# Performance work log

Hardware: AMD Instinct MI355X
Metric: run time of the kernel (lower is better)

The kernel has to match this reference:

```python
import jax, jax.numpy as jnp
import numpy as np

T, B, I, H, E, C = 256, 64, 1024, 1024, 4, 128
STDV = 1.0 / np.sqrt(H)


def setup_inputs() -> dict:
    key = jax.random.key(0)
    ks = jax.random.split(key, 8)
    x_seq = jax.random.normal(ks[0], (T, B, I), dtype=jnp.float32)
    h0 = jnp.zeros((1, B, H), dtype=jnp.float32)
    c0 = jnp.zeros((1, B, H), dtype=jnp.float32)
    coef = jax.random.uniform(ks[1], (B, E), dtype=jnp.float32)
    # expert params (uniform(-stdv, stdv) init as in the torch module)
    u = lambda k, shp: jax.random.uniform(k, shp, dtype=jnp.float32, minval=-STDV, maxval=STDV)
    Wi = u(ks[2], (E, 4 * H, I))
    bi = u(ks[3], (E, 4 * H))
    Wh = u(ks[4], (E, 4 * H, H))
    bh = u(ks[5], (E, 4 * H))
    Wo = u(ks[6], (E, C, H))
    bo = u(ks[7], (E, C))
    return {"x_seq": x_seq, "h0": h0, "c0": c0, "coef": coef,
            "Wi": Wi, "bi": bi, "Wh": Wh, "bh": bh, "Wo": Wo, "bo": bo}


def reference(x_seq, h0, c0, coef, Wi, bi, Wh, bh, Wo, bo):
    # MoO with IDGate == per-sample convex combination of expert linear outputs,
    # which equals a linear layer with per-sample mixed weights.
    # Precompute mixed input projections for all timesteps: [T,B,4H]
    xi = jnp.einsum('tbi,eoi,be->tbo', x_seq, Wi, coef) + coef @ bi
    # Per-sample mixed hidden weights: [B,4H,H] and bias [B,4H]
    Whm = jnp.einsum('eoi,be->boi', Wh, coef)
    bhm = coef @ bh

    def step(carry, xg):
        h, c = carry
        gates = xg + jnp.einsum('bi,boi->bo', h, Whm) + bhm  # [B,4H]
        ig, fg, gg, og = jnp.split(gates, 4, axis=-1)  # i,f,g,o order as in torch chunk
        c = jax.nn.sigmoid(fg) * c + jax.nn.sigmoid(ig) * jnp.tanh(gg)
        h = jax.nn.sigmoid(og) * jnp.tanh(c)
        return (h, c), h

    (hT, cT), hs = jax.lax.scan(step, (h0[0], c0[0]), xi)  # hs: [T,B,H]
    # h2o: mixed output projection (activation is identity, dropout p=0)
    out = jnp.einsum('tbh,ech,be->tbc', hs, Wo, coef) + coef @ bo  # [T,B,C]
    return out, hT[None], cT[None]
```

## Files before the change

kernel.cpp:

```cpp
#include <hip/hip_runtime.h>
#include <hip/hip_fp16.h>
#include <cstdint>

#define T_  256
#define B_  64
#define I_  1024
#define H_  1024
#define E_  4
#define C_  128
#define G4  4096

typedef _Float16 f16;
typedef _Float16 f16x2 __attribute__((ext_vector_type(2)));
typedef _Float16 f16x8 __attribute__((ext_vector_type(8)));
typedef float    f32x4 __attribute__((ext_vector_type(4)));

__device__ __forceinline__ float sigmoidf_(float x) { return 1.f / (1.f + __expf(-x)); }

union pk2 { uint32_t u; f16x2 h; };

__global__ void k_f32_to_f16(const float* __restrict__ src, f16* __restrict__ dst, int n8) {
    int i = blockIdx.x * blockDim.x + threadIdx.x;
    int stride = gridDim.x * blockDim.x;
    for (; i < n8; i += stride) {
        const float4* s = reinterpret_cast<const float4*>(src) + (size_t)i * 2;
        float4 a = s[0], b = s[1];
        f16x8 v = { (f16)a.x, (f16)a.y, (f16)a.z, (f16)a.w,
                    (f16)b.x, (f16)b.y, (f16)b.z, (f16)b.w };
        *reinterpret_cast<f16x8*>(dst + (size_t)i * 8) = v;
    }
}

__global__ void k_mix_biases(const float* __restrict__ coef, const float* __restrict__ bi,
                             const float* __restrict__ bh, const float* __restrict__ bo,
                             float* __restrict__ gbias, float* __restrict__ bom) {
    int idx = blockIdx.x * blockDim.x + threadIdx.x;
    int stride = gridDim.x * blockDim.x;
    for (int i = idx; i < B_ * G4; i += stride) {
        int b = i >> 12, o = i & (G4 - 1);
        float s = 0.f;
#pragma unroll
        for (int e = 0; e < 4; ++e) s += coef[b * 4 + e] * (bi[e * G4 + o] + bh[e * G4 + o]);
        gbias[i] = s;
    }
    for (int i = idx; i < B_ * C_; i += stride) {
        int b = i >> 7, c = i & (C_ - 1);
        float s = 0.f;
#pragma unroll
        for (int e = 0; e < 4; ++e) s += coef[b * 4 + e] * bo[e * C_ + c];
        bom[i] = s;
    }
}

__global__ void k_init_h0h(const float* __restrict__ h0, f16* __restrict__ h0h) {
    int i = blockIdx.x * blockDim.x + threadIdx.x;
    if (i < B_ * H_) h0h[i] = (f16)h0[i];
}

template<bool XF16, bool WF16>
__global__ __launch_bounds__(256, 1) void k_xi_gemm(
        const f16* __restrict__ xh, const float* __restrict__ xf,
        const f16* __restrict__ Wih, const float* __restrict__ Wif,
        const float* __restrict__ coef, const float* __restrict__ gbias,
        f16* __restrict__ xi) {
    __shared__ f16 As[256 * 72];
    __shared__ f16 Bs[128 * 72];
    const int nt = blockIdx.x;
    const int b  = blockIdx.y;
    const int tid = threadIdx.x;
    const int lane = tid & 63, wave = tid >> 6;
    const int wr = wave >> 1, wc = wave & 1;

    float cf[4];
#pragma unroll
    for (int e = 0; e < 4; ++e) cf[e] = coef[b * 4 + e];

    f32x4 acc[8][4];
#pragma unroll
    for (int mi = 0; mi < 8; ++mi)
#pragma unroll
        for (int ni = 0; ni < 4; ++ni) acc[mi][ni] = 0.f;

    for (int kk = 0; kk < I_; kk += 64) {
        __syncthreads();
#pragma unroll
        for (int it = 0; it < 8; ++it) {
            int chunk = it * 256 + tid;
            int row = chunk >> 3, c8 = chunk & 7;
            if constexpr (XF16) {
                *reinterpret_cast<f16x8*>(&As[row * 72 + c8 * 8]) =
                    *reinterpret_cast<const f16x8*>(&xh[((size_t)row * B_ + b) * I_ + kk + c8 * 8]);
            } else {
                const float4* p = reinterpret_cast<const float4*>(&xf[((size_t)row * B_ + b) * I_ + kk + c8 * 8]);
                float4 a = p[0], bq = p[1];
                f16x8 v = { (f16)a.x, (f16)a.y, (f16)a.z, (f16)a.w,
                            (f16)bq.x, (f16)bq.y, (f16)bq.z, (f16)bq.w };
                *reinterpret_cast<f16x8*>(&As[row * 72 + c8 * 8]) = v;
            }
        }
#pragma unroll
        for (int it = 0; it < 4; ++it) {
            int chunk = it * 256 + tid;
            int n = chunk >> 3, c8 = chunk & 7;
            if constexpr (WF16) {
                size_t base = ((size_t)(nt * 128 + n)) * I_ + kk + c8 * 8;
                f16 c0 = (f16)cf[0], c1 = (f16)cf[1], c2 = (f16)cf[2], c3 = (f16)cf[3];
                f16x8 w0 = *reinterpret_cast<const f16x8*>(&Wih[base]);
                f16x8 w1 = *reinterpret_cast<const f16x8*>(&Wih[base + (size_t)1 * G4 * I_]);
                f16x8 w2 = *reinterpret_cast<const f16x8*>(&Wih[base + (size_t)2 * G4 * I_]);
                f16x8 w3 = *reinterpret_cast<const f16x8*>(&Wih[base + (size_t)3 * G4 * I_]);
                f16x8 m = w0 * c0 + w1 * c1 + w2 * c2 + w3 * c3;
                *reinterpret_cast<f16x8*>(&Bs[n * 72 + c8 * 8]) = m;
            } else {
                size_t base = ((size_t)(nt * 128 + n)) * I_ + kk + c8 * 8;
                float m[8];
#pragma unroll
                for (int j = 0; j < 8; ++j) m[j] = 0.f;
#pragma unroll
                for (int e = 0; e < 4; ++e) {
                    const float4* p = reinterpret_cast<const float4*>(&Wif[base + (size_t)e * G4 * I_]);
                    float4 a = p[0], bq = p[1];
                    m[0] += cf[e] * a.x;  m[1] += cf[e] * a.y;
                    m[2] += cf[e] * a.z;  m[3] += cf[e] * a.w;
                    m[4] += cf[e] * bq.x; m[5] += cf[e] * bq.y;
                    m[6] += cf[e] * bq.z; m[7] += cf[e] * bq.w;
                }
                f16x8 v = { (f16)m[0], (f16)m[1], (f16)m[2], (f16)m[3],
                            (f16)m[4], (f16)m[5], (f16)m[6], (f16)m[7] };
                *reinterpret_cast<f16x8*>(&Bs[n * 72 + c8 * 8]) = v;
            }
        }
        __syncthreads();
#pragma unroll
        for (int ks = 0; ks < 2; ++ks) {
            int ko = ks * 32 + (lane >> 4) * 8;
            f16x8 a[8], bb[4];
#pragma unroll
            for (int mi = 0; mi < 8; ++mi)
                a[mi] = *reinterpret_cast<const f16x8*>(&As[(wr * 128 + mi * 16 + (lane & 15)) * 72 + ko]);
#pragma unroll
            for (int ni = 0; ni < 4; ++ni)
                bb[ni] = *reinterpret_cast<const f16x8*>(&Bs[(wc * 64 + ni * 16 + (lane & 15)) * 72 + ko]);
#pragma unroll
            for (int mi = 0; mi < 8; ++mi)
#pragma unroll
                for (int ni = 0; ni < 4; ++ni)
                    acc[mi][ni] = __builtin_amdgcn_mfma_f32_16x16x32_f16(a[mi], bb[ni], acc[mi][ni], 0, 0, 0);
        }
    }
#pragma unroll
    for (int mi = 0; mi < 8; ++mi)
#pragma unroll
        for (int ni = 0; ni < 4; ++ni)
#pragma unroll
            for (int j = 0; j < 4; ++j) {
                int t = wr * 128 + mi * 16 + (lane >> 4) * 4 + j;
                int o = nt * 128 + wc * 64 + ni * 16 + (lane & 15);
                float v = acc[mi][ni][j] + gbias[b * G4 + o];
                xi[((size_t)t * B_ + b) * G4 + o] = (f16)v;
            }
}

__device__ __forceinline__ void grid_barrier3(int* __restrict__ arr, int* __restrict__ go,
                                              int t, int bid) {
    __syncthreads();
    const int tid = threadIdx.x;
    if (bid == 0) {
        if (tid >= 1 && tid < 256) {
            while (__hip_atomic_load(&arr[t * 256 + tid], __ATOMIC_RELAXED,
                                     __HIP_MEMORY_SCOPE_AGENT) == 0)
                __builtin_amdgcn_s_sleep(1);
        }
        __syncthreads();
        if (tid == 0)
            __hip_atomic_store(&go[t * 512 + 511], 1, __ATOMIC_RELEASE,
                               __HIP_MEMORY_SCOPE_AGENT);
        __syncthreads();
        if (tid < 32)
            __hip_atomic_store(&go[t * 512 + tid * 16], 1, __ATOMIC_RELAXED,
                               __HIP_MEMORY_SCOPE_AGENT);
        __syncthreads();
    } else {
        if (tid == 0) {
            __hip_atomic_store(&arr[t * 256 + bid], 1, __ATOMIC_RELEASE,
                               __HIP_MEMORY_SCOPE_AGENT);
            while (__hip_atomic_load(&go[t * 512 + (bid >> 3) * 16], __ATOMIC_RELAXED,
                                     __HIP_MEMORY_SCOPE_AGENT) == 0)
                __builtin_amdgcn_s_sleep(1);
        }
        __builtin_amdgcn_sched_barrier(0);
        __syncthreads();
    }
}

#define POOL_SZ  148480
#define AS0_OFF  131072
#define AS1_OFF  (131072 + 8192)
#define GL_OFF   131072

#define BF(KC, KS) (*reinterpret_cast<const f16x8*>(pool + wrow + (KC) * 128 + (((KS) * 64 + koff) ^ swz)))

#define PRE(KC, PF) PF = *reinterpret_cast<const f16x8*>(&hprev[(size_t)sr * hstr + (KC) * 64 + soct * 8]);

#define AFR(AOFF, AROW, KS) (*reinterpret_cast<const f16x8*>(pool + (AOFF) + (AROW) + (((KS) * 64 + koff) ^ swz)))

#define MM4(ROFF) \
    acc0 = __builtin_amdgcn_mfma_f32_16x16x32_f16(AFR(ROFF, arow0, 0), bq0, acc0, 0, 0, 0); \
    acc1 = __builtin_amdgcn_mfma_f32_16x16x32_f16(AFR(ROFF, arow1, 0), bq0, acc1, 0, 0, 0); \
    acc0 = __builtin_amdgcn_mfma_f32_16x16x32_f16(AFR(ROFF, arow0, 1), bq1, acc0, 0, 0, 0); \
    acc1 = __builtin_amdgcn_mfma_f32_16x16x32_f16(AFR(ROFF, arow1, 1), bq1, acc1, 0, 0, 0);

#define KSTP(KC, ROFF, WOFF, PFW, PFL) { \
    const f16x8 bq0 = BF(KC, 0), bq1 = BF(KC, 1); \
    PRE((KC) + 8, PFL); \
    MM4(ROFF); \
    *reinterpret_cast<f16x8*>(pool + (WOFF) + sdst) = PFW; \
    __syncthreads(); \
}
#define KST(KC, ROFF, WOFF, PFW) { \
    const f16x8 bq0 = BF(KC, 0), bq1 = BF(KC, 1); \
    MM4(ROFF); \
    *reinterpret_cast<f16x8*>(pool + (WOFF) + sdst) = PFW; \
    __syncthreads(); \
}

__global__ __launch_bounds__(512, 1) void k_rec_persist(
        const float* __restrict__ Wh, const f16* __restrict__ h0h,
        const float* __restrict__ c0, f16* xi, const float* __restrict__ coef,
        float* __restrict__ out, int* __restrict__ arr, int* __restrict__ go) {
    __shared__ __attribute__((aligned(16))) char pool[POOL_SZ];
    float* gl = reinterpret_cast<float*>(pool + GL_OFF);

    const int bid = blockIdx.x;
    const int jb = ((bid & 7) << 5) | (bid >> 3);
    const int tid = threadIdx.x, lane = tid & 63, w = tid >> 6;
    const int ex = w & 3, mh = w >> 2;
    const int l15 = lane & 15, hi8 = (lane >> 4) * 8;

    for (int i = tid; i < 8192; i += 512) {
        int r = i >> 7, oct = i & 127;
        int e = r >> 4, g = (r >> 2) & 3, c = r & 3;
        const float* src = &Wh[((size_t)e * G4 + g * H_ + jb * 4 + c) * H_ + oct * 8];
        float4 f0 = *reinterpret_cast<const float4*>(src);
        float4 f1 = *reinterpret_cast<const float4*>(src + 4);
        f16x8 v = { (f16)f0.x, (f16)f0.y, (f16)f0.z, (f16)f0.w,
                    (f16)f1.x, (f16)f1.y, (f16)f1.z, (f16)f1.w };
        int db = r * 2048 + ((oct * 16) ^ ((r & 7) << 4));
        *reinterpret_cast<f16x8*>(pool + db) = v;
    }

    const int bb = tid >> 1, pr = tid & 1;
    const int cp0 = jb * 4 + pr * 2;
    float c_reg0 = 0.f, c_reg1 = 0.f;
    float4 cf4 = {0.f, 0.f, 0.f, 0.f};
    if (tid < 128) {
        c_reg0 = c0[bb * H_ + cp0];
        c_reg1 = c0[bb * H_ + cp0 + 1];
        cf4 = *reinterpret_cast<const float4*>(&coef[bb * 4]);
    }

    const int swz   = (l15 & 7) << 4;
    const int koff  = hi8 * 2;
    const int wrow  = (ex * 16 + l15) * 2048;
    const int arow0 = (mh * 32 + l15) * 128;
    const int arow1 = arow0 + 16 * 128;
    const int sr = tid >> 3, soct = tid & 7;
    const int sdst = sr * 128 + ((soct * 16) ^ ((sr & 7) << 4));

    __syncthreads();

    float xgc0a = 0.f, xgc0b = 0.f, xgc1a = 0.f, xgc1b = 0.f;
    float xgc2a = 0.f, xgc2b = 0.f, xgc3a = 0.f, xgc3b = 0.f;
    if (tid < 128) {
        const f16* xp = &xi[((size_t)0 * B_ + bb) * G4 + cp0];
        pk2 p0; p0.u = __hip_atomic_load(reinterpret_cast<const uint32_t*>(xp),
                                         __ATOMIC_RELAXED, __HIP_MEMORY_SCOPE_AGENT);
        xgc0a = (float)p0.h.x; xgc0b = (float)p0.h.y;
        f16x2 g1 = *reinterpret_cast<const f16x2*>(xp + H_);
        f16x2 g2 = *reinterpret_cast<const f16x2*>(xp + 2 * H_);
        f16x2 g3 = *reinterpret_cast<const f16x2*>(xp + 3 * H_);
        xgc1a = (float)g1.x; xgc1b = (float)g1.y;
        xgc2a = (float)g2.x; xgc2b = (float)g2.y;
        xgc3a = (float)g3.x; xgc3b = (float)g3.y;
    }

    for (int t = 0; t < T_; ++t) {
        const f16* hprev = (t == 0) ? h0h : (xi + (size_t)(t - 1) * B_ * G4);
        const size_t hstr = (t == 0) ? (size_t)H_ : (size_t)G4;

        f16x8 pfa, pfb, pfc, pfd, pfe, pff, pfg, pfh;
        PRE(0, pfa) PRE(1, pfb) PRE(2, pfc) PRE(3, pfd)
        PRE(4, pfe) PRE(5, pff) PRE(6, pfg) PRE(7, pfh)

        float xgn0a = 0.f, xgn0b = 0.f, xgn1a = 0.f, xgn1b = 0.f;
        float xgn2a = 0.f, xgn2b = 0.f, xgn3a = 0.f, xgn3b = 0.f;
        if (t + 1 < T_ && tid < 128) {
            const f16* xq = &xi[((size_t)(t + 1) * B_ + bb) * G4 + cp0];
            pk2 p0; p0.u = __hip_atomic_load(reinterpret_cast<const uint32_t*>(xq),
                                             __ATOMIC_RELAXED, __HIP_MEMORY_SCOPE_AGENT);
            xgn0a = (float)p0.h.x; xgn0b = (float)p0.h.y;
            f16x2 g1 = *reinterpret_cast<const f16x2*>(xq + H_);
            f16x2 g2 = *reinterpret_cast<const f16x2*>(xq + 2 * H_);
            f16x2 g3 = *reinterpret_cast<const f16x2*>(xq + 3 * H_);
            xgn1a = (float)g1.x; xgn1b = (float)g1.y;
            xgn2a = (float)g2.x; xgn2b = (float)g2.y;
            xgn3a = (float)g3.x; xgn3b = (float)g3.y;
        }

        *reinterpret_cast<f16x8*>(pool + AS0_OFF + sdst) = pfa;
        f32x4 acc0 = {0.f, 0.f, 0.f, 0.f}, acc1 = {0.f, 0.f, 0.f, 0.f};
        __syncthreads();

        KSTP(0,  AS0_OFF, AS1_OFF, pfb, pfa)
        KSTP(1,  AS1_OFF, AS0_OFF, pfc, pfb)
        KSTP(2,  AS0_OFF, AS1_OFF, pfd, pfc)
        KSTP(3,  AS1_OFF, AS0_OFF, pfe, pfd)
        KSTP(4,  AS0_OFF, AS1_OFF, pff, pfe)
        KSTP(5,  AS1_OFF, AS0_OFF, pfg, pff)
        KSTP(6,  AS0_OFF, AS1_OFF, pfh, pfg)
        KSTP(7,  AS1_OFF, AS0_OFF, pfa, pfh)
        KST(8,   AS0_OFF, AS1_OFF, pfb)
        KST(9,   AS1_OFF, AS0_OFF, pfc)
        KST(10,  AS0_OFF, AS1_OFF, pfd)
        KST(11,  AS1_OFF, AS0_OFF, pfe)
        KST(12,  AS0_OFF, AS1_OFF, pff)
        KST(13,  AS1_OFF, AS0_OFF, pfg)
        KST(14,  AS0_OFF, AS1_OFF, pfh)
        {
            const f16x8 bq0 = BF(15, 0), bq1 = BF(15, 1);
            MM4(AS1_OFF);
            __syncthreads();
        }

#pragma unroll
        for (int j = 0; j < 4; ++j) {
            int r0 = mh * 32 + (lane >> 4) * 4 + j;
            gl[(ex * 64 + r0) * 17 + l15]      = acc0[j];
            gl[(ex * 64 + r0 + 16) * 17 + l15] = acc1[j];
        }
        __syncthreads();

        if (tid < 128) {
            float ga[4], gb[4];
#pragma unroll
            for (int g = 0; g < 4; ++g) {
                int nn = g * 4 + pr * 2;
                ga[g] = cf4.x * gl[(0 * 64 + bb) * 17 + nn] +
                        cf4.y * gl[(1 * 64 + bb) * 17 + nn] +
                        cf4.z * gl[(2 * 64 + bb) * 17 + nn] +
                        cf4.w * gl[(3 * 64 + bb) * 17 + nn];
                gb[g] = cf4.x * gl[(0 * 64 + bb) * 17 + nn + 1] +
                        cf4.y * gl[(1 * 64 + bb) * 17 + nn + 1] +
                        cf4.z * gl[(2 * 64 + bb) * 17 + nn + 1] +
                        cf4.w * gl[(3 * 64 + bb) * 17 + nn + 1];
            }
            ga[0] += xgc0a; ga[1] += xgc1a; ga[2] += xgc2a; ga[3] += xgc3a;
            gb[0] += xgc0b; gb[1] += xgc1b; gb[2] += xgc2b; gb[3] += xgc3b;
            float cn0 = sigmoidf_(ga[1]) * c_reg0 + sigmoidf_(ga[0]) * tanhf(ga[2]);
            float hn0 = sigmoidf_(ga[3]) * tanhf(cn0);
            float cn1 = sigmoidf_(gb[1]) * c_reg1 + sigmoidf_(gb[0]) * tanhf(gb[2]);
            float hn1 = sigmoidf_(gb[3]) * tanhf(cn1);
            c_reg0 = cn0; c_reg1 = cn1;
            pk2 st; st.h.x = (f16)hn0; st.h.y = (f16)hn1;
            __hip_atomic_store(reinterpret_cast<uint32_t*>(&xi[((size_t)t * B_ + bb) * G4 + cp0]),
                               st.u, __ATOMIC_RELAXED, __HIP_MEMORY_SCOPE_AGENT);
            if (t == T_ - 1) {
                out[(size_t)T_ * B_ * C_ + bb * H_ + cp0]     = hn0;
                out[(size_t)T_ * B_ * C_ + bb * H_ + cp0 + 1] = hn1;
                out[(size_t)T_ * B_ * C_ + B_ * H_ + bb * H_ + cp0]     = cn0;
                out[(size_t)T_ * B_ * C_ + B_ * H_ + bb * H_ + cp0 + 1] = cn1;
            }
        }
        xgc0a = xgn0a; xgc0b = xgn0b; xgc1a = xgn1a; xgc1b = xgn1b;
        xgc2a = xgn2a; xgc2b = xgn2b; xgc3a = xgn3a; xgc3b = xgn3b;
        if (t != T_ - 1) grid_barrier3(arr, go, t, bid);
    }
}

__global__ __launch_bounds__(256, 1) void k_out_gemm(
        const f16* __restrict__ hs, const f16* __restrict__ Woh,
        const float* __restrict__ coef, const float* __restrict__ bom,
        float* __restrict__ out) {
    __shared__ f16 As[64 * 72];
    __shared__ f16 Bs[256 * 72];
    __shared__ float cfs[64][4];
    const int nt = blockIdx.x;
    const int t  = blockIdx.y;
    const int tid = threadIdx.x, lane = tid & 63, w = tid >> 6;
    cfs[tid >> 2][tid & 3] = coef[tid];

    f32x4 acc[4][4];
#pragma unroll
    for (int e = 0; e < 4; ++e)
#pragma unroll
        for (int mi = 0; mi < 4; ++mi) acc[e][mi] = 0.f;

    for (int kk = 0; kk < H_; kk += 64) {
        __syncthreads();
#pragma unroll
        for (int it = 0; it < 2; ++it) {
            int chunk = it * 256 + tid;
            int row = chunk >> 3, c8 = chunk & 7;
            *reinterpret_cast<f16x8*>(&As[row * 72 + c8 * 8]) =
                *reinterpret_cast<const f16x8*>(&hs[((size_t)t * B_ + row) * G4 + kk + c8 * 8]);
        }
#pragma unroll
        for (int it = 0; it < 8; ++it) {
            int chunk = it * 256 + tid;
            int r = chunk >> 3, c8 = chunk & 7;
            int e = r >> 6, nn = r & 63;
            size_t grow = (size_t)e * C_ + nt * 64 + nn;
            *reinterpret_cast<f16x8*>(&Bs[r * 72 + c8 * 8]) =
                *reinterpret_cast<const f16x8*>(&Woh[grow * H_ + kk + c8 * 8]);
        }
        __syncthreads();
#pragma unroll
        for (int ks = 0; ks < 2; ++ks) {
            int ko = ks * 32 + (lane >> 4) * 8;
            f16x8 a[4];
#pragma unroll
            for (int mi = 0; mi < 4; ++mi)
                a[mi] = *reinterpret_cast<const f16x8*>(&As[(mi * 16 + (lane & 15)) * 72 + ko]);
#pragma unroll
            for (int e = 0; e < 4; ++e) {
                f16x8 bf = *reinterpret_cast<const f16x8*>(&Bs[(e * 64 + w * 16 + (lane & 15)) * 72 + ko]);
#pragma unroll
                for (int mi = 0; mi < 4; ++mi)
                    acc[e][mi] = __builtin_amdgcn_mfma_f32_16x16x32_f16(a[mi], bf, acc[e][mi], 0, 0, 0);
            }
        }
    }
#pragma unroll
    for (int mi = 0; mi < 4; ++mi)
#pragma unroll
        for (int j = 0; j < 4; ++j) {
            int bb = mi * 16 + (lane >> 4) * 4 + j;
            int cc = nt * 64 + w * 16 + (lane & 15);
            float v = cfs[bb][0] * acc[0][mi][j] + cfs[bb][1] * acc[1][mi][j] +
                      cfs[bb][2] * acc[2][mi][j] + cfs[bb][3] * acc[3][mi][j];
            v += bom[bb * C_ + cc];
            out[((size_t)t * B_ + bb) * C_ + cc] = v;
        }
}

extern "C" void kernel_launch(void* const* d_in, const int* in_sizes, int n_in,
                              void* d_out, int out_size, void* d_ws, size_t ws_size,
                              hipStream_t stream) {
    const float* x    = (const float*)d_in[0];
    const float* h0   = (const float*)d_in[1];
    const float* c0   = (const float*)d_in[2];
    const float* coef = (const float*)d_in[3];
    const float* Wi   = (const float*)d_in[4];
    const float* bi   = (const float*)d_in[5];
    const float* Wh   = (const float*)d_in[6];
    const float* bh   = (const float*)d_in[7];
    const float* Wo   = (const float*)d_in[8];
    const float* bo   = (const float*)d_in[9];
    float* out = (float*)d_out;

    char* base = (char*)d_ws;
    size_t off = 0;
    auto carve = [&](size_t bytes) -> char* {
        char* r = base + off;
        off = (off + bytes + 255) & ~(size_t)255;
        return r;
    };
    const size_t SZ_XI  = (size_t)T_ * B_ * G4 * 2;
    const size_t SZ_WOH = (size_t)E_ * C_ * H_ * 2;
    const size_t SZ_ARR = (size_t)T_ * 256 * 4;
    const size_t SZ_GO  = (size_t)T_ * 512 * 4;
    const size_t SZ_WIH = (size_t)E_ * G4 * I_ * 2;
    const size_t SZ_XH  = (size_t)T_ * B_ * I_ * 2;

    f16*   xi     = (f16*)carve(SZ_XI);
    f16*   Woh    = (f16*)carve(SZ_WOH);
    f16*   h0h    = (f16*)carve((size_t)B_ * H_ * 2);
    float* gbias  = (float*)carve((size_t)B_ * G4 * 4);
    float* bom    = (float*)carve((size_t)B_ * C_ * 4);
    int*   arr    = (int*)carve(SZ_ARR);
    int*   go     = (int*)carve(SZ_GO);

    f16* Wih = nullptr;
    f16* xh  = nullptr;
    if (off + SZ_WIH + 256 <= ws_size) Wih = (f16*)carve(SZ_WIH);
    if (Wih && off + SZ_XH + 256 <= ws_size) xh = (f16*)carve(SZ_XH);
    (void)in_sizes; (void)n_in; (void)out_size;

    hipMemsetAsync(arr, 0, SZ_ARR, stream);
    hipMemsetAsync(go, 0, SZ_GO, stream);

    if (xh)  k_f32_to_f16<<<2048, 256, 0, stream>>>(x,  xh,  (T_ * B_ * I_) / 8);
    if (Wih) k_f32_to_f16<<<2048, 256, 0, stream>>>(Wi, Wih, (E_ * G4 * I_) / 8);
    k_f32_to_f16<<<512,  256, 0, stream>>>(Wo, Woh, (E_ * C_ * H_) / 8);
    k_mix_biases<<<512, 256, 0, stream>>>(coef, bi, bh, bo, gbias, bom);
    k_init_h0h<<<(B_ * H_ + 255) / 256, 256, 0, stream>>>(h0, h0h);

    dim3 gx(32, 64);
    if (xh)
        k_xi_gemm<true,  true ><<<gx, 256, 0, stream>>>(xh, nullptr, Wih, nullptr, coef, gbias, xi);
    else if (Wih)
        k_xi_gemm<false, true ><<<gx, 256, 0, stream>>>(nullptr, x, Wih, nullptr, coef, gbias, xi);
    else
        k_xi_gemm<false, false><<<gx, 256, 0, stream>>>(nullptr, x, nullptr, Wi, coef, gbias, xi);

    {
        void* args[] = { (void*)&Wh, (void*)&h0h, (void*)&c0, (void*)&xi,
                         (void*)&coef, (void*)&out, (void*)&arr, (void*)&go };
        hipLaunchCooperativeKernel((const void*)k_rec_persist, dim3(256), dim3(512),
                                   args, 0, stream);
    }

    dim3 go_(2, 256);
    k_out_gemm<<<go_, 256, 0, stream>>>(xi, Woh, coef, bom, out);
}
```

Baseline: 2.688 ms.

## Replace global grid barrier with per-tile dataflow flags polled during k-loop

Removes the centralized two-level grid barrier between timesteps. Each block now publishes its own arrival flag. The last block of each 16-block tile to see its whole tile complete raises per-tile go flags, replicated into 16 lines. Consumers wait only for the tiles covering the h chunks they are about to load, polling inside the k-loop so compute on early chunks overlaps with late producers. The prefetch depth shrinks from 8 to 4 chunks to match the staggered waits. This adds more flag traffic and memory-ordering risk, since relaxed atomics are used without explicit release/acquire fences.

```diff
diff --git a/kernel.cpp b/kernel.cpp
--- a/kernel.cpp
+++ b/kernel.cpp
@@ -161,47 +161,13 @@
             }
 }
 
-__device__ __forceinline__ void grid_barrier3(int* __restrict__ arr, int* __restrict__ go,
-                                              int t, int bid) {
-    __syncthreads();
-    const int tid = threadIdx.x;
-    if (bid == 0) {
-        if (tid >= 1 && tid < 256) {
-            while (__hip_atomic_load(&arr[t * 256 + tid], __ATOMIC_RELAXED,
-                                     __HIP_MEMORY_SCOPE_AGENT) == 0)
-                __builtin_amdgcn_s_sleep(1);
-        }
-        __syncthreads();
-        if (tid == 0)
-            __hip_atomic_store(&go[t * 512 + 511], 1, __ATOMIC_RELEASE,
-                               __HIP_MEMORY_SCOPE_AGENT);
-        __syncthreads();
-        if (tid < 32)
-            __hip_atomic_store(&go[t * 512 + tid * 16], 1, __ATOMIC_RELAXED,
-                               __HIP_MEMORY_SCOPE_AGENT);
-        __syncthreads();
-    } else {
-        if (tid == 0) {
-            __hip_atomic_store(&arr[t * 256 + bid], 1, __ATOMIC_RELEASE,
-                               __HIP_MEMORY_SCOPE_AGENT);
-            while (__hip_atomic_load(&go[t * 512 + (bid >> 3) * 16], __ATOMIC_RELAXED,
-                                     __HIP_MEMORY_SCOPE_AGENT) == 0)
-                __builtin_amdgcn_s_sleep(1);
-        }
-        __builtin_amdgcn_sched_barrier(0);
-        __syncthreads();
-    }
-}
-
 #define POOL_SZ  148480
 #define AS0_OFF  131072
 #define AS1_OFF  (131072 + 8192)
 #define GL_OFF   131072
 
 #define BF(KC, KS) (*reinterpret_cast<const f16x8*>(pool + wrow + (KC) * 128 + (((KS) * 64 + koff) ^ swz)))
-
 #define PRE(KC, PF) PF = *reinterpret_cast<const f16x8*>(&hprev[(size_t)sr * hstr + (KC) * 64 + soct * 8]);
-
 #define AFR(AOFF, AROW, KS) (*reinterpret_cast<const f16x8*>(pool + (AOFF) + (AROW) + (((KS) * 64 + koff) ^ swz)))
 
 #define MM4(ROFF) \
@@ -212,7 +178,7 @@
 
 #define KSTP(KC, ROFF, WOFF, PFW, PFL) { \
     const f16x8 bq0 = BF(KC, 0), bq1 = BF(KC, 1); \
-    PRE((KC) + 8, PFL); \
+    PRE((KC) + 4, PFL); \
     MM4(ROFF); \
     *reinterpret_cast<f16x8*>(pool + (WOFF) + sdst) = PFW; \
     __syncthreads(); \
@@ -224,10 +190,17 @@
     __syncthreads(); \
 }
 
+#define GO2IDX(T, KC, L) ((((size_t)(T) * 16 + (KC)) * 16 + (L)) * 16)
+
+__device__ __forceinline__ void pollgo(const int* p) {
+    while (__hip_atomic_load(p, __ATOMIC_RELAXED, __HIP_MEMORY_SCOPE_AGENT) == 0)
+        __builtin_amdgcn_s_sleep(1);
+}
+
 __global__ __launch_bounds__(512, 1) void k_rec_persist(
         const float* __restrict__ Wh, const f16* __restrict__ h0h,
         const float* __restrict__ c0, f16* xi, const float* __restrict__ coef,
-        float* __restrict__ out, int* __restrict__ arr, int* __restrict__ go) {
+        float* __restrict__ out, int* __restrict__ arr, int* __restrict__ go2) {
     __shared__ __attribute__((aligned(16))) char pool[POOL_SZ];
     float* gl = reinterpret_cast<float*>(pool + GL_OFF);
 
@@ -236,6 +209,8 @@
     const int tid = threadIdx.x, lane = tid & 63, w = tid >> 6;
     const int ex = w & 3, mh = w >> 2;
     const int l15 = lane & 15, hi8 = (lane >> 4) * 8;
+    const int myTile = jb >> 4;
+    const int goLine = bid & 15;
 
     for (int i = tid; i < 8192; i += 512) {
         int r = i >> 7, oct = i & 127;
@@ -288,9 +263,14 @@
         const f16* hprev = (t == 0) ? h0h : (xi + (size_t)(t - 1) * B_ * G4);
         const size_t hstr = (t == 0) ? (size_t)H_ : (size_t)G4;
 
-        f16x8 pfa, pfb, pfc, pfd, pfe, pff, pfg, pfh;
+        if (t > 0) {
+            if (tid < 8) pollgo(&go2[GO2IDX(t - 1, tid, goLine)]);
+            __builtin_amdgcn_sched_barrier(0);
+            __syncthreads();
+        }
+
+        f16x8 pfa, pfb, pfc, pfd;
         PRE(0, pfa) PRE(1, pfb) PRE(2, pfc) PRE(3, pfd)
-        PRE(4, pfe) PRE(5, pff) PRE(6, pfg) PRE(7, pfh)
 
         float xgn0a = 0.f, xgn0b = 0.f, xgn1a = 0.f, xgn1b = 0.f;
         float xgn2a = 0.f, xgn2b = 0.f, xgn3a = 0.f, xgn3b = 0.f;
@@ -311,21 +291,23 @@
         f32x4 acc0 = {0.f, 0.f, 0.f, 0.f}, acc1 = {0.f, 0.f, 0.f, 0.f};
         __syncthreads();
 
+        if (t > 0 && tid < 4) pollgo(&go2[GO2IDX(t - 1, 8 + tid, goLine)]);
         KSTP(0,  AS0_OFF, AS1_OFF, pfb, pfa)
         KSTP(1,  AS1_OFF, AS0_OFF, pfc, pfb)
         KSTP(2,  AS0_OFF, AS1_OFF, pfd, pfc)
-        KSTP(3,  AS1_OFF, AS0_OFF, pfe, pfd)
-        KSTP(4,  AS0_OFF, AS1_OFF, pff, pfe)
-        KSTP(5,  AS1_OFF, AS0_OFF, pfg, pff)
-        KSTP(6,  AS0_OFF, AS1_OFF, pfh, pfg)
-        KSTP(7,  AS1_OFF, AS0_OFF, pfa, pfh)
-        KST(8,   AS0_OFF, AS1_OFF, pfb)
-        KST(9,   AS1_OFF, AS0_OFF, pfc)
-        KST(10,  AS0_OFF, AS1_OFF, pfd)
-        KST(11,  AS1_OFF, AS0_OFF, pfe)
-        KST(12,  AS0_OFF, AS1_OFF, pff)
-        KST(13,  AS1_OFF, AS0_OFF, pfg)
-        KST(14,  AS0_OFF, AS1_OFF, pfh)
+        KSTP(3,  AS1_OFF, AS0_OFF, pfa, pfd)
+        if (t > 0 && tid < 4) pollgo(&go2[GO2IDX(t - 1, 12 + tid, goLine)]);
+        KSTP(4,  AS0_OFF, AS1_OFF, pfb, pfa)
+        KSTP(5,  AS1_OFF, AS0_OFF, pfc, pfb)
+        KSTP(6,  AS0_OFF, AS1_OFF, pfd, pfc)
+        KSTP(7,  AS1_OFF, AS0_OFF, pfa, pfd)
+        KSTP(8,  AS0_OFF, AS1_OFF, pfb, pfa)
+        KSTP(9,  AS1_OFF, AS0_OFF, pfc, pfb)
+        KSTP(10, AS0_OFF, AS1_OFF, pfd, pfc)
+        KSTP(11, AS1_OFF, AS0_OFF, pfa, pfd)
+        KST(12,  AS0_OFF, AS1_OFF, pfb)
+        KST(13,  AS1_OFF, AS0_OFF, pfc)
+        KST(14,  AS0_OFF, AS1_OFF, pfd)
         {
             const f16x8 bq0 = BF(15, 0), bq1 = BF(15, 1);
             MM4(AS1_OFF);
@@ -373,7 +355,24 @@
         }
         xgc0a = xgn0a; xgc0b = xgn0b; xgc1a = xgn1a; xgc1b = xgn1b;
         xgc2a = xgn2a; xgc2b = xgn2b; xgc3a = xgn3a; xgc3b = xgn3b;
-        if (t != T_ - 1) grid_barrier3(arr, go, t, bid);
+
+        if (t < T_ - 1) {
+            __syncthreads();
+            if (tid == 0)
+                __hip_atomic_store(&arr[t * 256 + jb], 1, __ATOMIC_RELAXED,
+                                   __HIP_MEMORY_SCOPE_AGENT);
+            __syncthreads();
+            if (tid < 64) {
+                int v = 1;
+                if (lane < 16)
+                    v = __hip_atomic_load(&arr[t * 256 + myTile * 16 + lane],
+                                          __ATOMIC_RELAXED, __HIP_MEMORY_SCOPE_AGENT);
+                unsigned long long m = __ballot(v != 0);
+                if (m == ~0ull && lane < 16)
+                    __hip_atomic_store(&go2[GO2IDX(t, myTile, lane)], 1,
+                                       __ATOMIC_RELAXED, __HIP_MEMORY_SCOPE_AGENT);
+            }
+        }
     }
 }
 
@@ -468,7 +467,7 @@
     const size_t SZ_XI  = (size_t)T_ * B_ * G4 * 2;
     const size_t SZ_WOH = (size_t)E_ * C_ * H_ * 2;
     const size_t SZ_ARR = (size_t)T_ * 256 * 4;
-    const size_t SZ_GO  = (size_t)T_ * 512 * 4;
+    const size_t SZ_GO2 = (size_t)T_ * 16 * 16 * 16 * 4;
     const size_t SZ_WIH = (size_t)E_ * G4 * I_ * 2;
     const size_t SZ_XH  = (size_t)T_ * B_ * I_ * 2;
 
@@ -478,7 +477,7 @@
     float* gbias  = (float*)carve((size_t)B_ * G4 * 4);
     float* bom    = (float*)carve((size_t)B_ * C_ * 4);
     int*   arr    = (int*)carve(SZ_ARR);
-    int*   go     = (int*)carve(SZ_GO);
+    int*   go2    = (int*)carve(SZ_GO2);
 
     f16* Wih = nullptr;
     f16* xh  = nullptr;
@@ -487,7 +486,7 @@
     (void)in_sizes; (void)n_in; (void)out_size;
 
     hipMemsetAsync(arr, 0, SZ_ARR, stream);
-    hipMemsetAsync(go, 0, SZ_GO, stream);
+    hipMemsetAsync(go2, 0, SZ_GO2, stream);
 
     if (xh)  k_f32_to_f16<<<2048, 256, 0, stream>>>(x,  xh,  (T_ * B_ * I_) / 8);
     if (Wih) k_f32_to_f16<<<2048, 256, 0, stream>>>(Wi, Wih, (E_ * G4 * I_) / 8);
@@ -505,7 +504,7 @@
 
     {
         void* args[] = { (void*)&Wh, (void*)&h0h, (void*)&c0, (void*)&xi,
-                         (void*)&coef, (void*)&out, (void*)&arr, (void*)&go };
+                         (void*)&coef, (void*)&out, (void*)&arr, (void*)&go2 };
         hipLaunchCooperativeKernel((const void*)k_rec_persist, dim3(256), dim3(512),
                                    args, 0, stream);
     }
```

Measured after the change: 2.316 ms. 13.8% less time.
